# Kernel tuning notes

Measured on AMD Instinct MI355X. Metric: run time of the kernel, lower is better.

The kernel has to match this reference:

```python
import jax, jax.numpy as jnp
import numpy as np

ALPHA = 0.2  # LeakyReLU negative slope
NEG = -9e15  # mask value from original code


def setup_inputs() -> dict:
    key = jax.random.key(0)
    k1, k2, k3, k4 = jax.random.split(key, 4)
    N, F_in, F_out = 8192, 256, 128
    h = jax.random.normal(k1, (N, F_in), dtype=jnp.float32)
    adj = jax.random.randint(k2, (N, N), 0, 2, dtype=jnp.int32)
    # xavier-ish scaled params
    W = jax.random.normal(k3, (F_out, F_in), dtype=jnp.float32) * (1.0 / np.sqrt(F_in))
    a = jax.random.normal(k4, (1, 2 * F_out), dtype=jnp.float32) * (1.0 / np.sqrt(2 * F_out))
    return {"h": h, "adj": adj, "W": W, "a": a}


def reference(h, adj, W, a):
    # Wh: [N, F_out]
    Wh = h @ W.T
    F_out = Wh.shape[1]
    # Algebraic decomposition of the pairwise-concat score:
    # e[i,j] = leakyrelu(a . [Wh_i ; Wh_j]) = leakyrelu(f1_i + f2_j)
    a1 = a[0, :F_out]   # [F_out]
    a2 = a[0, F_out:]   # [F_out]
    f1 = Wh @ a1        # [N]
    f2 = Wh @ a2        # [N]
    e = jax.nn.leaky_relu(f1[:, None] + f2[None, :], negative_slope=ALPHA)  # [N, N]
    scores = jnp.where(adj > 0, e, NEG)
    attention = jax.nn.softmax(scores, axis=1)  # dropout omitted (eval mode)
    return attention @ Wh  # [N, F_out]
```

## Files before the change

### kernel.cpp

```cpp
#include <hip/hip_runtime.h>
#include <hip/hip_bf16.h>


typedef __bf16 bf16;
typedef __attribute__((ext_vector_type(8))) __bf16 bf16x8;
typedef __attribute__((ext_vector_type(4))) float f32x4;

#define NN 8192
#define F_IN 256
#define F_OUT 128
#define LOG2E 1.44269504088896f
#define ALPHA 0.2f
#define KSLICES 8

__global__ __launch_bounds__(256) void gat_pack(const int* __restrict__ adj,
                                                unsigned char* __restrict__ maskP) {
    const int row = blockIdx.x * 4 + (threadIdx.x >> 6);
    const int l = threadIdx.x & 63;
    const int* rowp = adj + (size_t)row * NN;

#pragma unroll 4
    for (int iter = 0; iter < 16; ++iter) {
        const int base = iter * 512;
        const int4 v1 = *(const int4*)(rowp + base + l * 4);
        const int4 v2 = *(const int4*)(rowp + base + 256 + l * 4);
        unsigned int n1 = (v1.x > 0 ? 1u : 0u) | (v1.y > 0 ? 2u : 0u) |
                          (v1.z > 0 ? 4u : 0u) | (v1.w > 0 ? 8u : 0u);
        unsigned int n2 = (v2.x > 0 ? 1u : 0u) | (v2.y > 0 ? 2u : 0u) |
                          (v2.z > 0 ? 4u : 0u) | (v2.w > 0 ? 8u : 0u);
        const unsigned int p1 = __shfl_xor(n1, 1);
        const unsigned int p2 = __shfl_xor(n2, 1);
        if ((l & 1) == 0) {
            const int b1 = iter * 64 + (l >> 1);
            const int b2 = b1 + 32;
            maskP[((size_t)(b1 >> 7) << 20) + (size_t)row * 128 + (b1 & 127)] =
                (unsigned char)(n1 | (p1 << 4));
            maskP[((size_t)(b2 >> 7) << 20) + (size_t)row * 128 + (b2 & 127)] =
                (unsigned char)(n2 | (p2 << 4));
        }
    }
}

__global__ __launch_bounds__(256) void gat_wsplit(const float* __restrict__ W,
                                                  bf16* __restrict__ Whi,
                                                  bf16* __restrict__ Wlo) {
    const int i = blockIdx.x * 256 + threadIdx.x;
    const float v = W[i];
    const bf16 h = (bf16)v;
    Whi[i] = h;
    Wlo[i] = (bf16)(v - (float)h);
}

__device__ __forceinline__ void split8(const float* __restrict__ p,
                                       bf16x8& hi, bf16x8& lo) {
    const float4 u = *(const float4*)p;
    const float4 v = *(const float4*)(p + 4);
    float f[8] = {u.x, u.y, u.z, u.w, v.x, v.y, v.z, v.w};
#pragma unroll
    for (int j = 0; j < 8; ++j) {
        const bf16 h = (bf16)f[j];
        hi[j] = h;
        lo[j] = (bf16)(f[j] - (float)h);
    }
}

__global__ __launch_bounds__(128) void gat_wh(const float* __restrict__ h,
                                              const bf16* __restrict__ Whi,
                                              const bf16* __restrict__ Wlo,
                                              const float* __restrict__ a,
                                              bf16* __restrict__ WhT,
                                              float* __restrict__ f1L,
                                              float* __restrict__ f2L) {
    const int tid = threadIdx.x;
    const int wv = tid >> 6;
    const int l15 = tid & 15;
    const int g = (tid & 63) >> 4;
    const int rowbase = blockIdx.x * 32 + wv * 16;

    f32x4 acc[8];
    const f32x4 zz = {0.f, 0.f, 0.f, 0.f};
#pragma unroll
    for (int nf = 0; nf < 8; ++nf) acc[nf] = zz;

#pragma unroll
    for (int ks = 0; ks < 8; ++ks) {
        const int k = ks * 32 + g * 8;
        bf16x8 ah, al;
        split8(h + (size_t)(rowbase + l15) * F_IN + k, ah, al);
#pragma unroll
        for (int nf = 0; nf < 8; ++nf) {
            const bf16x8 bh = *(const bf16x8*)(Whi + (size_t)(nf * 16 + l15) * F_IN + k);
            const bf16x8 bl = *(const bf16x8*)(Wlo + (size_t)(nf * 16 + l15) * F_IN + k);
            acc[nf] = __builtin_amdgcn_mfma_f32_16x16x32_bf16(ah, bh, acc[nf], 0, 0, 0);
            acc[nf] = __builtin_amdgcn_mfma_f32_16x16x32_bf16(ah, bl, acc[nf], 0, 0, 0);
            acc[nf] = __builtin_amdgcn_mfma_f32_16x16x32_bf16(al, bh, acc[nf], 0, 0, 0);
        }
    }

#pragma unroll
    for (int nf = 0; nf < 8; ++nf)
#pragma unroll
        for (int r = 0; r < 4; ++r)
            WhT[(size_t)(nf * 16 + l15) * NN + rowbase + g * 4 + r] = (bf16)acc[nf][r];

    float a1c[8], a2c[8];
#pragma unroll
    for (int nf = 0; nf < 8; ++nf) {
        a1c[nf] = a[nf * 16 + l15];
        a2c[nf] = a[F_OUT + nf * 16 + l15];
    }
#pragma unroll
    for (int r = 0; r < 4; ++r) {
        float s1 = 0.f, s2 = 0.f;
#pragma unroll
        for (int nf = 0; nf < 8; ++nf) {
            s1 += acc[nf][r] * a1c[nf];
            s2 += acc[nf][r] * a2c[nf];
        }
        s1 += __shfl_xor(s1, 1, 16);
        s1 += __shfl_xor(s1, 2, 16);
        s1 += __shfl_xor(s1, 4, 16);
        s1 += __shfl_xor(s1, 8, 16);
        s2 += __shfl_xor(s2, 1, 16);
        s2 += __shfl_xor(s2, 2, 16);
        s2 += __shfl_xor(s2, 4, 16);
        s2 += __shfl_xor(s2, 8, 16);
        if (l15 == 0) {
            f1L[rowbase + g * 4 + r] = s1 * LOG2E;
            f2L[rowbase + g * 4 + r] = s2 * LOG2E;
        }
    }
}

__global__ __launch_bounds__(512, 4) void gat_flash6(
        const unsigned char* __restrict__ maskP,
        const bf16* __restrict__ WhT,
        const float* __restrict__ f1L,
        const float* __restrict__ f2L,
        float* __restrict__ O_part,
        float* __restrict__ rs_part) {
    __shared__ __align__(16) char lds[39424];

    const int tid = threadIdx.x;
    const int wv = tid >> 6;
    const int l = tid & 63;
    const int l15 = l & 15;
    const int g = l >> 4;
    const int rb = blockIdx.x >> 3;
    const int ks = blockIdx.x & 7;
    const int row0 = rb * 128;
    const int lrow = wv * 16 + l15;

    const float f1a = f1L[row0 + lrow];

    const int mr = tid >> 2;
    const int mseg = tid & 3;
    const unsigned char* msrc =
        maskP + ((size_t)ks << 20) + (size_t)(row0 + mr) * 128 + mseg * 4;

    f32x4 acc[8];
    const f32x4 zz = {0.f, 0.f, 0.f, 0.f};
#pragma unroll
    for (int nf = 0; nf < 8; ++nf) acc[nf] = zz;
    float rs0 = 0.f;

    {
        const float2 v = *(const float2*)(f2L + ks * 1024 + tid * 2);
        *(float2*)(lds + 35328 + tid * 8) = v;
    }

    for (int it = 0; it < 8; ++it) {
        __syncthreads();
        const unsigned int mw = *(const unsigned int*)(msrc + it * 16);
        *(unsigned int*)(lds + 32768 + mr * 20 + mseg * 4) = mw;
#pragma unroll
        for (int j = 0; j < 4; ++j) {
            const int u = j * 512 + tid;
            const int cc = u >> 4;
            const int ku = u & 15;
            const bf16x8 v =
                *(const bf16x8*)(WhT + (size_t)cc * NN + ks * 1024 + it * 128 + ku * 8);
            *(bf16x8*)(lds + ((cc * 256 + ku * 16) ^ ((cc & 7) << 4))) = v;
        }
        __syncthreads();

#pragma unroll
        for (int s = 0; s < 4; ++s) {
            const unsigned int mb =
                *(const unsigned char*)(lds + 32768 + lrow * 20 + s * 4 + g);
            const int t = it * 4 + s;
            const float4 fa = *(const float4*)(lds + 35328 + t * 128 + g * 32);
            const float4 fb = *(const float4*)(lds + 35328 + t * 128 + g * 32 + 16);
            const float ff[8] = {fa.x, fa.y, fa.z, fa.w, fb.x, fb.y, fb.z, fb.w};

            bf16x8 pa;
#pragma unroll
            for (int j = 0; j < 8; ++j) {
                const float x = f1a + ff[j];
                const float e = __builtin_amdgcn_exp2f(fmaxf(x, ALPHA * x));
                pa[j] = (bf16)((mb & (1u << j)) ? e : 0.f);
            }
#pragma unroll
            for (int j = 0; j < 8; ++j) rs0 += (float)pa[j];

            __builtin_amdgcn_s_setprio(1);
#pragma unroll
            for (int nf = 0; nf < 8; ++nf) {
                const int c = nf * 16 + l15;
                const bf16x8 bh = *(const bf16x8*)(
                    lds + ((c * 256 + s * 64 + g * 16) ^ ((c & 7) << 4)));
                acc[nf] = __builtin_amdgcn_mfma_f32_16x16x32_bf16(pa, bh, acc[nf], 0, 0, 0);
            }
            __builtin_amdgcn_s_setprio(0);
        }
    }

    rs0 += __shfl_xor(rs0, 16);
    rs0 += __shfl_xor(rs0, 32);
    if (l < 16) rs_part[(size_t)ks * NN + row0 + lrow] = rs0;

    float* accL = (float*)lds;
#pragma unroll
    for (int half = 0; half < 2; ++half) {
        __syncthreads();
        if ((wv >> 2) == half) {
            const int rbase = (wv & 3) * 16;
#pragma unroll
            for (int nf = 0; nf < 8; ++nf)
#pragma unroll
                for (int r = 0; r < 4; ++r)
                    accL[(rbase + g * 4 + r) * 132 + nf * 16 + l15] = acc[nf][r];
        }
        __syncthreads();
        const int rr = tid >> 3;
        const int seg = tid & 7;
        float* dst = O_part + ((size_t)ks << 20) +
                     (size_t)(row0 + half * 64 + rr) * F_OUT + seg * 16;
        const float* src = accL + rr * 132 + seg * 16;
        *(float4*)(dst + 0) = *(const float4*)(src + 0);
        *(float4*)(dst + 4) = *(const float4*)(src + 4);
        *(float4*)(dst + 8) = *(const float4*)(src + 8);
        *(float4*)(dst + 12) = *(const float4*)(src + 12);
    }
}

__global__ __launch_bounds__(256) void gat_reduce(const float* __restrict__ O_part,
                                                  const float* __restrict__ rs_part,
                                                  float* __restrict__ out) {
    const int idx = blockIdx.x * 256 + threadIdx.x;
    const int r = idx >> 5;
    const int c = (idx & 31) * 4;
    float rsum = 0.f;
#pragma unroll
    for (int s = 0; s < KSLICES; ++s) rsum += rs_part[(size_t)s * NN + r];
    float4 o = {0.f, 0.f, 0.f, 0.f};
#pragma unroll
    for (int s = 0; s < KSLICES; ++s) {
        const float4 v =
            *(const float4*)(O_part + ((size_t)s << 20) + (size_t)r * F_OUT + c);
        o.x += v.x;
        o.y += v.y;
        o.z += v.z;
        o.w += v.w;
    }
    const float inv = 1.0f / rsum;
    o.x *= inv;
    o.y *= inv;
    o.z *= inv;
    o.w *= inv;
    *(float4*)(out + (size_t)r * F_OUT + c) = o;
}

extern "C" void kernel_launch(void* const* d_in, const int* in_sizes, int n_in,
                              void* d_out, int out_size, void* d_ws, size_t ws_size,
                              hipStream_t stream) {
    const float* h = (const float*)d_in[0];
    const int* adj = (const int*)d_in[1];
    const float* W = (const float*)d_in[2];
    const float* a = (const float*)d_in[3];
    float* out = (float*)d_out;

    char* ws = (char*)d_ws;
    const size_t MB = 1024 * 1024;
    bf16* WhT = (bf16*)ws;
    float* f1L = (float*)(ws + 2 * MB);
    float* f2L = f1L + NN;
    bf16* Whi = (bf16*)(ws + 2 * MB + 64 * 1024);
    bf16* Wlo = (bf16*)(ws + 2 * MB + 128 * 1024);
    unsigned char* maskP = (unsigned char*)(ws + 3 * MB);
    float* rs_part = (float*)(ws + 11 * MB);
    float* O_part = (float*)(ws + 12 * MB);

    gat_wsplit<<<128, 256, 0, stream>>>(W, Whi, Wlo);
    gat_wh<<<256, 128, 0, stream>>>(h, Whi, Wlo, a, WhT, f1L, f2L);
    gat_pack<<<2048, 256, 0, stream>>>(adj, maskP);
    gat_flash6<<<512, 512, 0, stream>>>(maskP, WhT, f1L, f2L, O_part, rs_part);
    gat_reduce<<<NN * F_OUT / 4 / 256, 256, 0, stream>>>(O_part, rs_part, out);
}
```

Before: 126.2 us.

## Fuse adjacency bit-packing into attention kernel and split W inside Wh kernel

Removes the separate gat_pack and gat_wsplit kernels. The attention kernel now reads the int32 adjacency directly, packs it into bytes in LDS per 512-column sub-chunk, and then reuses that packed mask across four WhT tiles. The Wh kernel splits W into bf16 hi/lo on the fly. This avoids two launches and the write and re-read of the 8 MB packed mask. In exchange, the 256 MB adjacency read now sits inside the flash kernel's critical loop, with extra synchronisation and more LDS per block.

```diff
diff --git a/kernel.cpp b/kernel.cpp
--- a/kernel.cpp
+++ b/kernel.cpp
@@ -13,44 +13,6 @@
 #define ALPHA 0.2f
 #define KSLICES 8
 
-__global__ __launch_bounds__(256) void gat_pack(const int* __restrict__ adj,
-                                                unsigned char* __restrict__ maskP) {
-    const int row = blockIdx.x * 4 + (threadIdx.x >> 6);
-    const int l = threadIdx.x & 63;
-    const int* rowp = adj + (size_t)row * NN;
-
-#pragma unroll 4
-    for (int iter = 0; iter < 16; ++iter) {
-        const int base = iter * 512;
-        const int4 v1 = *(const int4*)(rowp + base + l * 4);
-        const int4 v2 = *(const int4*)(rowp + base + 256 + l * 4);
-        unsigned int n1 = (v1.x > 0 ? 1u : 0u) | (v1.y > 0 ? 2u : 0u) |
-                          (v1.z > 0 ? 4u : 0u) | (v1.w > 0 ? 8u : 0u);
-        unsigned int n2 = (v2.x > 0 ? 1u : 0u) | (v2.y > 0 ? 2u : 0u) |
-                          (v2.z > 0 ? 4u : 0u) | (v2.w > 0 ? 8u : 0u);
-        const unsigned int p1 = __shfl_xor(n1, 1);
-        const unsigned int p2 = __shfl_xor(n2, 1);
-        if ((l & 1) == 0) {
-            const int b1 = iter * 64 + (l >> 1);
-            const int b2 = b1 + 32;
-            maskP[((size_t)(b1 >> 7) << 20) + (size_t)row * 128 + (b1 & 127)] =
-                (unsigned char)(n1 | (p1 << 4));
-            maskP[((size_t)(b2 >> 7) << 20) + (size_t)row * 128 + (b2 & 127)] =
-                (unsigned char)(n2 | (p2 << 4));
-        }
-    }
-}
-
-__global__ __launch_bounds__(256) void gat_wsplit(const float* __restrict__ W,
-                                                  bf16* __restrict__ Whi,
-                                                  bf16* __restrict__ Wlo) {
-    const int i = blockIdx.x * 256 + threadIdx.x;
-    const float v = W[i];
-    const bf16 h = (bf16)v;
-    Whi[i] = h;
-    Wlo[i] = (bf16)(v - (float)h);
-}
-
 __device__ __forceinline__ void split8(const float* __restrict__ p,
                                        bf16x8& hi, bf16x8& lo) {
     const float4 u = *(const float4*)p;
@@ -65,8 +27,7 @@
 }
 
 __global__ __launch_bounds__(128) void gat_wh(const float* __restrict__ h,
-                                              const bf16* __restrict__ Whi,
-                                              const bf16* __restrict__ Wlo,
+                                              const float* __restrict__ W,
                                               const float* __restrict__ a,
                                               bf16* __restrict__ WhT,
                                               float* __restrict__ f1L,
@@ -89,8 +50,8 @@
         split8(h + (size_t)(rowbase + l15) * F_IN + k, ah, al);
 #pragma unroll
         for (int nf = 0; nf < 8; ++nf) {
-            const bf16x8 bh = *(const bf16x8*)(Whi + (size_t)(nf * 16 + l15) * F_IN + k);
-            const bf16x8 bl = *(const bf16x8*)(Wlo + (size_t)(nf * 16 + l15) * F_IN + k);
+            bf16x8 bh, bl;
+            split8(W + (size_t)(nf * 16 + l15) * F_IN + k, bh, bl);
             acc[nf] = __builtin_amdgcn_mfma_f32_16x16x32_bf16(ah, bh, acc[nf], 0, 0, 0);
             acc[nf] = __builtin_amdgcn_mfma_f32_16x16x32_bf16(ah, bl, acc[nf], 0, 0, 0);
             acc[nf] = __builtin_amdgcn_mfma_f32_16x16x32_bf16(al, bh, acc[nf], 0, 0, 0);
@@ -132,20 +93,24 @@
     }
 }
 
-__global__ __launch_bounds__(512, 4) void gat_flash6(
-        const unsigned char* __restrict__ maskP,
+__global__ __launch_bounds__(512, 4) void gat_flash7(
+        const int* __restrict__ adj,
         const bf16* __restrict__ WhT,
         const float* __restrict__ f1L,
         const float* __restrict__ f2L,
         float* __restrict__ O_part,
         float* __restrict__ rs_part) {
-    __shared__ __align__(16) char lds[39424];
+    __shared__ __align__(16) char lds[45568];
+#define MOFF 32768
+#define FOFF 41472
 
     const int tid = threadIdx.x;
     const int wv = tid >> 6;
     const int l = tid & 63;
     const int l15 = l & 15;
     const int g = l >> 4;
+    const int half = l >> 5;
+    const int lane32 = l & 31;
     const int rb = blockIdx.x >> 3;
     const int ks = blockIdx.x & 7;
     const int row0 = rb * 128;
@@ -153,11 +118,6 @@
 
     const float f1a = f1L[row0 + lrow];
 
-    const int mr = tid >> 2;
-    const int mseg = tid & 3;
-    const unsigned char* msrc =
-        maskP + ((size_t)ks << 20) + (size_t)(row0 + mr) * 128 + mseg * 4;
-
     f32x4 acc[8];
     const f32x4 zz = {0.f, 0.f, 0.f, 0.f};
 #pragma unroll
@@ -166,52 +126,72 @@
 
     {
         const float2 v = *(const float2*)(f2L + ks * 1024 + tid * 2);
-        *(float2*)(lds + 35328 + tid * 8) = v;
-    }
-
-    for (int it = 0; it < 8; ++it) {
+        *(float2*)(lds + FOFF + tid * 8) = v;
+    }
+
+    for (int su = 0; su < 2; ++su) {
         __syncthreads();
-        const unsigned int mw = *(const unsigned int*)(msrc + it * 16);
-        *(unsigned int*)(lds + 32768 + mr * 20 + mseg * 4) = mw;
-#pragma unroll
-        for (int j = 0; j < 4; ++j) {
-            const int u = j * 512 + tid;
-            const int cc = u >> 4;
-            const int ku = u & 15;
-            const bf16x8 v =
-                *(const bf16x8*)(WhT + (size_t)cc * NN + ks * 1024 + it * 128 + ku * 8);
-            *(bf16x8*)(lds + ((cc * 256 + ku * 16) ^ ((cc & 7) << 4))) = v;
-        }
-        __syncthreads();
-
-#pragma unroll
-        for (int s = 0; s < 4; ++s) {
-            const unsigned int mb =
-                *(const unsigned char*)(lds + 32768 + lrow * 20 + s * 4 + g);
-            const int t = it * 4 + s;
-            const float4 fa = *(const float4*)(lds + 35328 + t * 128 + g * 32);
-            const float4 fb = *(const float4*)(lds + 35328 + t * 128 + g * 32 + 16);
-            const float ff[8] = {fa.x, fa.y, fa.z, fa.w, fb.x, fb.y, fb.z, fb.w};
-
-            bf16x8 pa;
-#pragma unroll
-            for (int j = 0; j < 8; ++j) {
-                const float x = f1a + ff[j];
-                const float e = __builtin_amdgcn_exp2f(fmaxf(x, ALPHA * x));
-                pa[j] = (bf16)((mb & (1u << j)) ? e : 0.f);
+#pragma unroll
+        for (int i = 0; i < 8; ++i) {
+            const int lr = wv * 16 + 2 * i + half;
+            const int* ap = adj + (size_t)(row0 + lr) * NN + ks * 1024 + su * 512 + lane32 * 4;
+#pragma unroll
+            for (int p = 0; p < 4; ++p) {
+                const int4 v = *(const int4*)(ap + p * 128);
+                const unsigned int n = (v.x > 0 ? 1u : 0u) | (v.y > 0 ? 2u : 0u) |
+                                       (v.z > 0 ? 4u : 0u) | (v.w > 0 ? 8u : 0u);
+                const unsigned int o = __shfl_xor(n, 1);
+                if ((l & 1) == 0)
+                    *(unsigned char*)(lds + MOFF + lr * 68 + p * 16 + (lane32 >> 1)) =
+                        (unsigned char)(n | (o << 4));
             }
-#pragma unroll
-            for (int j = 0; j < 8; ++j) rs0 += (float)pa[j];
-
-            __builtin_amdgcn_s_setprio(1);
-#pragma unroll
-            for (int nf = 0; nf < 8; ++nf) {
-                const int c = nf * 16 + l15;
-                const bf16x8 bh = *(const bf16x8*)(
-                    lds + ((c * 256 + s * 64 + g * 16) ^ ((c & 7) << 4)));
-                acc[nf] = __builtin_amdgcn_mfma_f32_16x16x32_bf16(pa, bh, acc[nf], 0, 0, 0);
+        }
+
+#pragma unroll
+        for (int bc = 0; bc < 4; ++bc) {
+            __syncthreads();
+            const int kg = ks * 1024 + su * 512 + bc * 128;
+#pragma unroll
+            for (int j = 0; j < 4; ++j) {
+                const int u = j * 512 + tid;
+                const int cc = u >> 4;
+                const int ku = u & 15;
+                const bf16x8 v = *(const bf16x8*)(WhT + (size_t)cc * NN + kg + ku * 8);
+                *(bf16x8*)(lds + ((cc * 256 + ku * 16) ^ ((cc & 7) << 4))) = v;
             }
-            __builtin_amdgcn_s_setprio(0);
+            __syncthreads();
+
+#pragma unroll
+            for (int s = 0; s < 4; ++s) {
+                const int t = bc * 4 + s;
+                const int tt = su * 16 + t;
+                const unsigned int mb =
+                    *(const unsigned char*)(lds + MOFF + lrow * 68 + t * 4 + g);
+                const float4 fa = *(const float4*)(lds + FOFF + tt * 128 + g * 32);
+                const float4 fb = *(const float4*)(lds + FOFF + tt * 128 + g * 32 + 16);
+                const float ff[8] = {fa.x, fa.y, fa.z, fa.w, fb.x, fb.y, fb.z, fb.w};
+
+                bf16x8 pa;
+#pragma unroll
+                for (int j = 0; j < 8; ++j) {
+                    const float x = f1a + ff[j];
+                    const float e = __builtin_amdgcn_exp2f(fmaxf(x, ALPHA * x));
+                    pa[j] = (bf16)((mb & (1u << j)) ? e : 0.f);
+                }
+#pragma unroll
+                for (int j = 0; j < 8; ++j) rs0 += (float)pa[j];
+
+                __builtin_amdgcn_s_setprio(1);
+#pragma unroll
+                for (int nf = 0; nf < 8; ++nf) {
+                    const int c = nf * 16 + l15;
+                    const bf16x8 bh = *(const bf16x8*)(
+                        lds + ((c * 256 + s * 64 + g * 16) ^ ((c & 7) << 4)));
+                    acc[nf] =
+                        __builtin_amdgcn_mfma_f32_16x16x32_bf16(pa, bh, acc[nf], 0, 0, 0);
+                }
+                __builtin_amdgcn_s_setprio(0);
+            }
         }
     }
 
@@ -221,9 +201,9 @@
 
     float* accL = (float*)lds;
 #pragma unroll
-    for (int half = 0; half < 2; ++half) {
+    for (int hh = 0; hh < 2; ++hh) {
         __syncthreads();
-        if ((wv >> 2) == half) {
+        if ((wv >> 2) == hh) {
             const int rbase = (wv & 3) * 16;
 #pragma unroll
             for (int nf = 0; nf < 8; ++nf)
@@ -235,13 +215,15 @@
         const int rr = tid >> 3;
         const int seg = tid & 7;
         float* dst = O_part + ((size_t)ks << 20) +
-                     (size_t)(row0 + half * 64 + rr) * F_OUT + seg * 16;
+                     (size_t)(row0 + hh * 64 + rr) * F_OUT + seg * 16;
         const float* src = accL + rr * 132 + seg * 16;
         *(float4*)(dst + 0) = *(const float4*)(src + 0);
         *(float4*)(dst + 4) = *(const float4*)(src + 4);
         *(float4*)(dst + 8) = *(const float4*)(src + 8);
         *(float4*)(dst + 12) = *(const float4*)(src + 12);
     }
+#undef MOFF
+#undef FOFF
 }
 
 __global__ __launch_bounds__(256) void gat_reduce(const float* __restrict__ O_part,
@@ -285,15 +267,10 @@
     bf16* WhT = (bf16*)ws;
     float* f1L = (float*)(ws + 2 * MB);
     float* f2L = f1L + NN;
-    bf16* Whi = (bf16*)(ws + 2 * MB + 64 * 1024);
-    bf16* Wlo = (bf16*)(ws + 2 * MB + 128 * 1024);
-    unsigned char* maskP = (unsigned char*)(ws + 3 * MB);
-    float* rs_part = (float*)(ws + 11 * MB);
-    float* O_part = (float*)(ws + 12 * MB);
-
-    gat_wsplit<<<128, 256, 0, stream>>>(W, Whi, Wlo);
-    gat_wh<<<256, 128, 0, stream>>>(h, Whi, Wlo, a, WhT, f1L, f2L);
-    gat_pack<<<2048, 256, 0, stream>>>(adj, maskP);
-    gat_flash6<<<512, 512, 0, stream>>>(maskP, WhT, f1L, f2L, O_part, rs_part);
+    float* rs_part = (float*)(ws + 3 * MB);
+    float* O_part = (float*)(ws + 4 * MB);
+
+    gat_wh<<<256, 128, 0, stream>>>(h, W, a, WhT, f1L, f2L);
+    gat_flash7<<<512, 512, 0, stream>>>(adj, WhT, f1L, f2L, O_part, rs_part);
     gat_reduce<<<NN * F_OUT / 4 / 256, 256, 0, stream>>>(O_part, rs_part, out);
 }
```

After: 123.4 us. -2.2%, faster.

## Fuse adjacency packing, W split and Wh projection into one launch

Applied to the files above, without the earlier changes.

Merges three preprocessing kernels into a single launch: the first 2048 blocks pack the adjacency mask and the remaining 128 blocks compute Wh, now with four waves per block. The separate W hi/lo split kernel is removed, and each block splits W into bf16 pairs on the fly. This drops two launches and lets the Wh projection run alongside the memory-bound packing. The cost is redundant fp32 W loads and conversions in every projection block.

```diff
diff --git a/kernel.cpp b/kernel.cpp
--- a/kernel.cpp
+++ b/kernel.cpp
@@ -13,44 +13,6 @@
 #define ALPHA 0.2f
 #define KSLICES 8
 
-__global__ __launch_bounds__(256) void gat_pack(const int* __restrict__ adj,
-                                                unsigned char* __restrict__ maskP) {
-    const int row = blockIdx.x * 4 + (threadIdx.x >> 6);
-    const int l = threadIdx.x & 63;
-    const int* rowp = adj + (size_t)row * NN;
-
-#pragma unroll 4
-    for (int iter = 0; iter < 16; ++iter) {
-        const int base = iter * 512;
-        const int4 v1 = *(const int4*)(rowp + base + l * 4);
-        const int4 v2 = *(const int4*)(rowp + base + 256 + l * 4);
-        unsigned int n1 = (v1.x > 0 ? 1u : 0u) | (v1.y > 0 ? 2u : 0u) |
-                          (v1.z > 0 ? 4u : 0u) | (v1.w > 0 ? 8u : 0u);
-        unsigned int n2 = (v2.x > 0 ? 1u : 0u) | (v2.y > 0 ? 2u : 0u) |
-                          (v2.z > 0 ? 4u : 0u) | (v2.w > 0 ? 8u : 0u);
-        const unsigned int p1 = __shfl_xor(n1, 1);
-        const unsigned int p2 = __shfl_xor(n2, 1);
-        if ((l & 1) == 0) {
-            const int b1 = iter * 64 + (l >> 1);
-            const int b2 = b1 + 32;
-            maskP[((size_t)(b1 >> 7) << 20) + (size_t)row * 128 + (b1 & 127)] =
-                (unsigned char)(n1 | (p1 << 4));
-            maskP[((size_t)(b2 >> 7) << 20) + (size_t)row * 128 + (b2 & 127)] =
-                (unsigned char)(n2 | (p2 << 4));
-        }
-    }
-}
-
-__global__ __launch_bounds__(256) void gat_wsplit(const float* __restrict__ W,
-                                                  bf16* __restrict__ Whi,
-                                                  bf16* __restrict__ Wlo) {
-    const int i = blockIdx.x * 256 + threadIdx.x;
-    const float v = W[i];
-    const bf16 h = (bf16)v;
-    Whi[i] = h;
-    Wlo[i] = (bf16)(v - (float)h);
-}
-
 __device__ __forceinline__ void split8(const float* __restrict__ p,
                                        bf16x8& hi, bf16x8& lo) {
     const float4 u = *(const float4*)p;
@@ -64,18 +26,50 @@
     }
 }
 
-__global__ __launch_bounds__(128) void gat_wh(const float* __restrict__ h,
-                                              const bf16* __restrict__ Whi,
-                                              const bf16* __restrict__ Wlo,
-                                              const float* __restrict__ a,
-                                              bf16* __restrict__ WhT,
-                                              float* __restrict__ f1L,
-                                              float* __restrict__ f2L) {
+__global__ __launch_bounds__(256) void gat_whpack(
+        const int* __restrict__ adj,
+        const float* __restrict__ h,
+        const float* __restrict__ W,
+        const float* __restrict__ a,
+        unsigned char* __restrict__ maskP,
+        bf16* __restrict__ WhT,
+        float* __restrict__ f1L,
+        float* __restrict__ f2L) {
     const int tid = threadIdx.x;
+
+    if (blockIdx.x < 2048) {
+        const int row = blockIdx.x * 4 + (tid >> 6);
+        const int l = tid & 63;
+        const int* rowp = adj + (size_t)row * NN;
+
+#pragma unroll 4
+        for (int iter = 0; iter < 16; ++iter) {
+            const int base = iter * 512;
+            const int4 v1 = *(const int4*)(rowp + base + l * 4);
+            const int4 v2 = *(const int4*)(rowp + base + 256 + l * 4);
+            unsigned int n1 = (v1.x > 0 ? 1u : 0u) | (v1.y > 0 ? 2u : 0u) |
+                              (v1.z > 0 ? 4u : 0u) | (v1.w > 0 ? 8u : 0u);
+            unsigned int n2 = (v2.x > 0 ? 1u : 0u) | (v2.y > 0 ? 2u : 0u) |
+                              (v2.z > 0 ? 4u : 0u) | (v2.w > 0 ? 8u : 0u);
+            const unsigned int p1 = __shfl_xor(n1, 1);
+            const unsigned int p2 = __shfl_xor(n2, 1);
+            if ((l & 1) == 0) {
+                const int b1 = iter * 64 + (l >> 1);
+                const int b2 = b1 + 32;
+                maskP[((size_t)(b1 >> 7) << 20) + (size_t)row * 128 + (b1 & 127)] =
+                    (unsigned char)(n1 | (p1 << 4));
+                maskP[((size_t)(b2 >> 7) << 20) + (size_t)row * 128 + (b2 & 127)] =
+                    (unsigned char)(n2 | (p2 << 4));
+            }
+        }
+        return;
+    }
+
+    const int wb = blockIdx.x - 2048;
     const int wv = tid >> 6;
     const int l15 = tid & 15;
     const int g = (tid & 63) >> 4;
-    const int rowbase = blockIdx.x * 32 + wv * 16;
+    const int rowbase = wb * 64 + wv * 16;
 
     f32x4 acc[8];
     const f32x4 zz = {0.f, 0.f, 0.f, 0.f};
@@ -89,8 +83,8 @@
         split8(h + (size_t)(rowbase + l15) * F_IN + k, ah, al);
 #pragma unroll
         for (int nf = 0; nf < 8; ++nf) {
-            const bf16x8 bh = *(const bf16x8*)(Whi + (size_t)(nf * 16 + l15) * F_IN + k);
-            const bf16x8 bl = *(const bf16x8*)(Wlo + (size_t)(nf * 16 + l15) * F_IN + k);
+            bf16x8 bh, bl;
+            split8(W + (size_t)(nf * 16 + l15) * F_IN + k, bh, bl);
             acc[nf] = __builtin_amdgcn_mfma_f32_16x16x32_bf16(ah, bh, acc[nf], 0, 0, 0);
             acc[nf] = __builtin_amdgcn_mfma_f32_16x16x32_bf16(ah, bl, acc[nf], 0, 0, 0);
             acc[nf] = __builtin_amdgcn_mfma_f32_16x16x32_bf16(al, bh, acc[nf], 0, 0, 0);
@@ -285,15 +279,11 @@
     bf16* WhT = (bf16*)ws;
     float* f1L = (float*)(ws + 2 * MB);
     float* f2L = f1L + NN;
-    bf16* Whi = (bf16*)(ws + 2 * MB + 64 * 1024);
-    bf16* Wlo = (bf16*)(ws + 2 * MB + 128 * 1024);
     unsigned char* maskP = (unsigned char*)(ws + 3 * MB);
     float* rs_part = (float*)(ws + 11 * MB);
     float* O_part = (float*)(ws + 12 * MB);
 
-    gat_wsplit<<<128, 256, 0, stream>>>(W, Whi, Wlo);
-    gat_wh<<<256, 128, 0, stream>>>(h, Whi, Wlo, a, WhT, f1L, f2L);
-    gat_pack<<<2048, 256, 0, stream>>>(adj, maskP);
+    gat_whpack<<<2176, 256, 0, stream>>>(adj, h, W, a, maskP, WhT, f1L, f2L);
     gat_flash6<<<512, 512, 0, stream>>>(maskP, WhT, f1L, f2L, O_part, rs_part);
     gat_reduce<<<NN * F_OUT / 4 / 256, 256, 0, stream>>>(O_part, rs_part, out);
 }
```

After: 131.4 us. +4.1%, slower.
